# Optimization experiments

Measured on AMD Instinct MI355X. Metric: run time of the kernel, lower is better.

The kernel has to match this reference:

```python
import jax, jax.numpy as jnp
import numpy as np
import math

NUM_CLASSES = 100000
EMBED = 384
BATCH = 512
S = 64.0
M = 0.5
COS_M = math.cos(M)
SIN_M = math.sin(M)
TH = math.cos(math.pi - M)
MM = math.sin(math.pi - M) * M
EPS = 1e-07


def setup_inputs() -> dict:
    key = jax.random.key(0)
    k1, k2, k3 = jax.random.split(key, 3)
    embeddings = jax.random.normal(k1, (BATCH, EMBED), dtype=jnp.float32)
    labels = jax.random.randint(k2, (BATCH,), 0, NUM_CLASSES, dtype=jnp.int64)
    # xavier_uniform-like init for weight [num_classes, embedding_size]
    limit = math.sqrt(6.0 / (NUM_CLASSES + EMBED))
    weight = jax.random.uniform(k3, (NUM_CLASSES, EMBED), dtype=jnp.float32,
                                minval=-limit, maxval=limit)
    return {"embeddings": embeddings, "labels": labels, "weight": weight}


def reference(embeddings, labels, weight):
    # normalize class weights (note: embeddings are NOT normalized, per source)
    W = weight / jnp.linalg.norm(weight, axis=1, keepdims=True)  # [C, E]
    cos_theta = jnp.clip(embeddings @ W.T, -1.0 + EPS, 1.0 - EPS)  # [B, C]
    sin_theta = jnp.sqrt(1.0 - cos_theta ** 2)
    cos_theta_m = cos_theta * COS_M - sin_theta * SIN_M
    cos_theta_m = jnp.where(cos_theta > TH, cos_theta_m, cos_theta - MM)
    one_hot = jax.nn.one_hot(labels, cos_theta.shape[1], dtype=cos_theta.dtype)
    logits = S * (one_hot * cos_theta_m + (1.0 - one_hot) * cos_theta)
    # mean cross-entropy
    logp = jax.nn.log_softmax(logits, axis=-1)  # [B, C]
    nll = -jnp.take_along_axis(logp, labels[:, None], axis=1)[:, 0]
    return jnp.mean(nll)
```

## Files before the change

### kernel.cpp

```cpp
#include <hip/hip_runtime.h>
#include <hip/hip_bf16.h>
#include <math.h>

#define C_CLASSES 100000
#define EMBED     384
#define BATCH     512
#define S_SCALE   64.0f
#define COS_M_    0.8775825618903728f
#define SIN_M_    0.479425538604203f
#define TH_       (-0.8775825618903728f)
#define MM_       0.2397127693021015f
#define EPS_      1e-7f
#define LOG2E_    1.4426950408889634f
#define LN2_      0.6931471805599453f
#define BIGZ_     92.33261191693459f
#define SK1_      92.33248f

#define CT    160
#define NCH   625

typedef __attribute__((ext_vector_type(8))) short bf16x8;
typedef __attribute__((ext_vector_type(4))) float f32x4;

__device__ inline ushort f2bf(float f) {
    unsigned u = __float_as_uint(f);
    unsigned r = (u + 0x7fffu + ((u >> 16) & 1u)) >> 16;
    return (ushort)r;
}

__device__ inline ushort cvt_bf(float f) {
    __hip_bfloat16 h = __float2bfloat16(f);
    return *(ushort*)&h;
}

__global__ __launch_bounds__(256)
void cvt_pack_e(const float* __restrict__ emb, ushort* __restrict__ eP)
{
    int t = blockIdx.x * 256 + threadIdx.x;
    int lane = t & 63;
    int grp  = t >> 6;
    int tile = grp / 12, ks = grp % 12;
    int lr = lane & 15, lg = lane >> 4;
    int row = tile * 16 + lr;
    int col = ks * 32 + lg * 8;
    const float4* src = (const float4*)(emb + (size_t)row * EMBED + col);
    float4 v0 = src[0], v1 = src[1];
    ushort4 o0, o1;
    o0.x = f2bf(v0.x); o0.y = f2bf(v0.y); o0.z = f2bf(v0.z); o0.w = f2bf(v0.w);
    o1.x = f2bf(v1.x); o1.y = f2bf(v1.y); o1.z = f2bf(v1.z); o1.w = f2bf(v1.w);
    ((ushort4*)eP)[t * 2]     = o0;
    ((ushort4*)eP)[t * 2 + 1] = o1;
}

__global__ __launch_bounds__(1024, 4)
void arc_fused160(const ushort* __restrict__ eP, const int* __restrict__ labels,
                  const float* __restrict__ weight,
                  float* __restrict__ psum, float* __restrict__ zlabel)
{
    __shared__ ushort Bl[(CT / 16) * 12 * 512];
    __shared__ int    labL[BATCH];

    const int tid = threadIdx.x;

    const int orig = blockIdx.x;
    const int xcd  = orig & 7;
    const int qq   = NCH >> 3, rr = NCH & 7;
    const int blk  = (xcd < rr ? xcd * (qq + 1)
                               : rr * (qq + 1) + (xcd - rr) * qq) + (orig >> 3);
    const int c0   = blk * CT;

    if (tid < BATCH) labL[tid] = labels[tid];

    {
        const int p = tid & 15;
        #pragma unroll
        for (int h = 0; h < 3; ++h) {
            if (h < 2 || tid < 512) {
                const int c = h * 64 + (tid >> 4);
                const float4* src =
                    (const float4*)(weight + (size_t)(c0 + c) * EMBED) + p;

                float4 wv[6];
                float ss = 0.f;
                #pragma unroll
                for (int i = 0; i < 6; ++i) {
                    wv[i] = src[16 * i];
                    ss += wv[i].x * wv[i].x + wv[i].y * wv[i].y
                        + wv[i].z * wv[i].z + wv[i].w * wv[i].w;
                }
                ss += __shfl_xor(ss, 1, 64);
                ss += __shfl_xor(ss, 2, 64);
                ss += __shfl_xor(ss, 4, 64);
                ss += __shfl_xor(ss, 8, 64);
                const float inv = (ss > 0.f) ? rsqrtf(ss) : 0.f;

                const int t2 = c >> 4, cl = c & 15;
                #pragma unroll
                for (int i = 0; i < 6; ++i) {
                    int q   = p + 16 * i;
                    int ks  = q >> 3;
                    int lgp = (q >> 1) & 3;
                    int jo  = (q & 1) * 4;
                    ushort4 o;
                    o.x = cvt_bf(wv[i].x * inv); o.y = cvt_bf(wv[i].y * inv);
                    o.z = cvt_bf(wv[i].z * inv); o.w = cvt_bf(wv[i].w * inv);
                    int ei = (((t2 * 12 + ks) * 64) + cl + 16 * lgp) * 8 + jo;
                    ei ^= (lgp & 3) << 4;
                    *(ushort4*)&Bl[ei] = o;
                }
            }
            __builtin_amdgcn_sched_barrier(0);
        }
    }
    __syncthreads();

    const int wid = tid >> 6, l = tid & 63;
    const int lr  = l & 15,  lg = l >> 4;
    const int bxo = (lg & 3) << 4;

    const ushort* abase = eP + ((size_t)(wid * 2) * 12 * 64 + l) * 8;

    f32x4 acc[2][10];
    #pragma unroll
    for (int mt = 0; mt < 2; ++mt)
        #pragma unroll
        for (int nt = 0; nt < 10; ++nt)
            acc[mt][nt] = (f32x4){0.f, 0.f, 0.f, 0.f};

    #pragma unroll
    for (int ks = 0; ks < 12; ++ks) {
        bf16x8 a0 = *(const bf16x8*)(abase + (0 * 12 + ks) * 512);
        bf16x8 a1 = *(const bf16x8*)(abase + (1 * 12 + ks) * 512);
        #pragma unroll
        for (int nt = 0; nt < 10; ++nt) {
            int ei = ((nt * 12 + ks) * 64 + l) * 8;
            bf16x8 b = *(const bf16x8*)&Bl[ei ^ bxo];
            acc[0][nt] = __builtin_amdgcn_mfma_f32_16x16x32_bf16(
                a0, b, acc[0][nt], 0, 0, 0);
            acc[1][nt] = __builtin_amdgcn_mfma_f32_16x16x32_bf16(
                a1, b, acc[1][nt], 0, 0, 0);
        }
    }

    #pragma unroll
    for (int mt = 0; mt < 2; ++mt) {
        #pragma unroll
        for (int rg = 0; rg < 4; ++rg) {
            const int r   = wid * 32 + mt * 16 + lg * 4 + rg;
            const int lab = labL[r];
            float acc4 = 0.f;
            #pragma unroll
            for (int nt = 0; nt < 10; ++nt) {
                float cv = __builtin_amdgcn_fmed3f(acc[mt][nt][rg],
                                                   -1.f + EPS_, 1.f - EPS_);
                acc4 += exp2f(fmaf(cv, SK1_, -BIGZ_));
            }
            int off = lab - c0;
            if (((unsigned)off < (unsigned)CT) && ((off & 15) == lr)) {
                int ntl = off >> 4;
                float cv = acc[mt][0][rg];
                #pragma unroll
                for (int nt = 1; nt < 10; ++nt)
                    cv = (ntl == nt) ? acc[mt][nt][rg] : cv;
                cv = __builtin_amdgcn_fmed3f(cv, -1.f + EPS_, 1.f - EPS_);
                float plain = exp2f(fmaf(cv, SK1_, -BIGZ_));
                float zm;
                if (cv > TH_) {
                    float sv = sqrtf(fmaxf(1.f - cv * cv, 0.f));
                    zm = S_SCALE * (cv * COS_M_ - sv * SIN_M_);
                } else {
                    zm = S_SCALE * (cv - MM_);
                }
                acc4 += exp2f(fmaf(zm, LOG2E_, -BIGZ_)) - plain;
                zlabel[r] = zm;
            }
            acc4 += __shfl_xor(acc4, 1, 64);
            acc4 += __shfl_xor(acc4, 2, 64);
            acc4 += __shfl_xor(acc4, 4, 64);
            acc4 += __shfl_xor(acc4, 8, 64);
            if (lr == 0) psum[(size_t)blk * BATCH + r] = acc4;
        }
    }
}

__global__ __launch_bounds__(256)
void arc_reduce(const float* __restrict__ psum, const float* __restrict__ zlabel,
                float* __restrict__ rowloss)
{
    const int r = blockIdx.x;
    const int tid = threadIdx.x;
    float s = 0.f;
    for (int k = tid; k < NCH; k += 256)
        s += psum[(size_t)k * BATCH + r];
    #pragma unroll
    for (int d = 1; d < 64; d <<= 1) s += __shfl_xor(s, d, 64);
    __shared__ float ssh[4];
    if ((tid & 63) == 0) ssh[tid >> 6] = s;
    __syncthreads();
    if (tid == 0) {
        float t = ssh[0] + ssh[1] + ssh[2] + ssh[3];
        rowloss[r] = LN2_ * (BIGZ_ + log2f(t)) - zlabel[r];
    }
}

__global__ __launch_bounds__(512)
void arc_mean(const float* __restrict__ rowloss, float* __restrict__ out)
{
    const int tid = threadIdx.x;
    float v = rowloss[tid];
    #pragma unroll
    for (int d = 1; d < 64; d <<= 1) v += __shfl_xor(v, d, 64);
    __shared__ float sv[8];
    if ((tid & 63) == 0) sv[tid >> 6] = v;
    __syncthreads();
    if (tid == 0) {
        float t = 0.f;
        #pragma unroll
        for (int w = 0; w < 8; ++w) t += sv[w];
        out[0] = t / (float)BATCH;
    }
}

extern "C" void kernel_launch(void* const* d_in, const int* in_sizes, int n_in,
                              void* d_out, int out_size, void* d_ws, size_t ws_size,
                              hipStream_t stream)
{
    (void)in_sizes; (void)n_in; (void)out_size; (void)ws_size;
    const float* emb    = (const float*)d_in[0];
    const int*   labels = (const int*)d_in[1];
    const float* weight = (const float*)d_in[2];
    float* out = (float*)d_out;

    float*  psum    = (float*)d_ws;
    float*  zlabel  = psum + (size_t)NCH * BATCH;
    float*  rowloss = zlabel + BATCH;
    ushort* eP      = (ushort*)(rowloss + BATCH);

    cvt_pack_e<<<(BATCH * EMBED / 8) / 256, 256, 0, stream>>>(emb, eP);
    arc_fused160<<<NCH, 1024, 0, stream>>>(eP, labels, weight, psum, zlabel);
    arc_reduce<<<BATCH, 256, 0, stream>>>(psum, zlabel, rowloss);
    arc_mean<<<1, 512, 0, stream>>>(rowloss, out);
}
```

Before: 84.67 us.

## Retile per-wave MFMA work to 64 rows by 80 classes with split partial sums

Each of the 16 waves now computes a 64x80 tile (4 M-tiles by 5 N-tiles) instead of 32x160 (2 by 10). Each LDS B fragment is reused across four A fragments, which halves LDS reads per MFMA. The cost is twice as many global A loads per wave. The split over classes doubles the partial-sum buffer, so the reduce kernel now reads twice as many partials per row.

```diff
diff --git a/kernel.cpp b/kernel.cpp
--- a/kernel.cpp
+++ b/kernel.cpp
@@ -115,52 +115,57 @@
     __syncthreads();
 
     const int wid = tid >> 6, l = tid & 63;
+    const int mg  = wid & 7;
+    const int nh  = wid >> 3;
     const int lr  = l & 15,  lg = l >> 4;
     const int bxo = (lg & 3) << 4;
 
-    const ushort* abase = eP + ((size_t)(wid * 2) * 12 * 64 + l) * 8;
-
-    f32x4 acc[2][10];
-    #pragma unroll
-    for (int mt = 0; mt < 2; ++mt)
-        #pragma unroll
-        for (int nt = 0; nt < 10; ++nt)
+    const ushort* abase = eP + ((size_t)(mg * 4) * 12 * 64 + l) * 8;
+
+    f32x4 acc[4][5];
+    #pragma unroll
+    for (int mt = 0; mt < 4; ++mt)
+        #pragma unroll
+        for (int nt = 0; nt < 5; ++nt)
             acc[mt][nt] = (f32x4){0.f, 0.f, 0.f, 0.f};
 
     #pragma unroll
     for (int ks = 0; ks < 12; ++ks) {
-        bf16x8 a0 = *(const bf16x8*)(abase + (0 * 12 + ks) * 512);
-        bf16x8 a1 = *(const bf16x8*)(abase + (1 * 12 + ks) * 512);
-        #pragma unroll
-        for (int nt = 0; nt < 10; ++nt) {
-            int ei = ((nt * 12 + ks) * 64 + l) * 8;
+        bf16x8 a[4];
+        #pragma unroll
+        for (int mt = 0; mt < 4; ++mt)
+            a[mt] = *(const bf16x8*)(abase + (mt * 12 + ks) * 512);
+        #pragma unroll
+        for (int nt = 0; nt < 5; ++nt) {
+            int ei = (((nh * 5 + nt) * 12 + ks) * 64 + l) * 8;
             bf16x8 b = *(const bf16x8*)&Bl[ei ^ bxo];
-            acc[0][nt] = __builtin_amdgcn_mfma_f32_16x16x32_bf16(
-                a0, b, acc[0][nt], 0, 0, 0);
-            acc[1][nt] = __builtin_amdgcn_mfma_f32_16x16x32_bf16(
-                a1, b, acc[1][nt], 0, 0, 0);
+            #pragma unroll
+            for (int mt = 0; mt < 4; ++mt)
+                acc[mt][nt] = __builtin_amdgcn_mfma_f32_16x16x32_bf16(
+                    a[mt], b, acc[mt][nt], 0, 0, 0);
         }
     }
 
-    #pragma unroll
-    for (int mt = 0; mt < 2; ++mt) {
+    const int cbase = c0 + nh * 80;
+    #pragma unroll
+    for (int mt = 0; mt < 4; ++mt) {
         #pragma unroll
         for (int rg = 0; rg < 4; ++rg) {
-            const int r   = wid * 32 + mt * 16 + lg * 4 + rg;
+            const int r   = mg * 64 + mt * 16 + lg * 4 + rg;
             const int lab = labL[r];
             float acc4 = 0.f;
             #pragma unroll
-            for (int nt = 0; nt < 10; ++nt) {
+            for (int nt = 0; nt < 5; ++nt) {
                 float cv = __builtin_amdgcn_fmed3f(acc[mt][nt][rg],
                                                    -1.f + EPS_, 1.f - EPS_);
                 acc4 += exp2f(fmaf(cv, SK1_, -BIGZ_));
             }
-            int off = lab - c0;
-            if (((unsigned)off < (unsigned)CT) && ((off & 15) == lr)) {
+            int off = lab - cbase;
+            if (((unsigned)off < 80u) && ((off & 15) == lr)) {
                 int ntl = off >> 4;
                 float cv = acc[mt][0][rg];
                 #pragma unroll
-                for (int nt = 1; nt < 10; ++nt)
+                for (int nt = 1; nt < 5; ++nt)
                     cv = (ntl == nt) ? acc[mt][nt][rg] : cv;
                 cv = __builtin_amdgcn_fmed3f(cv, -1.f + EPS_, 1.f - EPS_);
                 float plain = exp2f(fmaf(cv, SK1_, -BIGZ_));
@@ -178,7 +183,8 @@
             acc4 += __shfl_xor(acc4, 2, 64);
             acc4 += __shfl_xor(acc4, 4, 64);
             acc4 += __shfl_xor(acc4, 8, 64);
-            if (lr == 0) psum[(size_t)blk * BATCH + r] = acc4;
+            if (lr == 0)
+                psum[((size_t)blk * 2 + nh) * BATCH + r] = acc4;
         }
     }
 }
@@ -190,7 +196,7 @@
     const int r = blockIdx.x;
     const int tid = threadIdx.x;
     float s = 0.f;
-    for (int k = tid; k < NCH; k += 256)
+    for (int k = tid; k < 2 * NCH; k += 256)
         s += psum[(size_t)k * BATCH + r];
     #pragma unroll
     for (int d = 1; d < 64; d <<= 1) s += __shfl_xor(s, d, 64);
@@ -232,7 +238,7 @@
     float* out = (float*)d_out;
 
     float*  psum    = (float*)d_ws;
-    float*  zlabel  = psum + (size_t)NCH * BATCH;
+    float*  zlabel  = psum + (size_t)2 * NCH * BATCH;
     float*  rowloss = zlabel + BATCH;
     ushort* eP      = (ushort*)(rowloss + BATCH);
 
```

After: 121.1 us. +43.1%, slower.

## Pipeline weight loading with MFMA passes over class-tile groups

Applied to the files above, without the earlier changes.

Splits the 160-class tile into three groups of 64/64/32 classes. While the MFMA pass runs on the group already staged in LDS, the next group's weights are loaded from global memory and then normalised and packed afterward, with a barrier between stages. The aim is to hide weight-load latency behind matrix compute instead of loading all weights before any MFMA work starts. The cost is extra barriers, shorter MFMA passes and register pressure from holding prefetched weights alongside the accumulators.

```diff
diff --git a/kernel.cpp b/kernel.cpp
--- a/kernel.cpp
+++ b/kernel.cpp
@@ -52,93 +52,77 @@
     ((ushort4*)eP)[t * 2 + 1] = o1;
 }
 
-__global__ __launch_bounds__(1024, 4)
-void arc_fused160(const ushort* __restrict__ eP, const int* __restrict__ labels,
-                  const float* __restrict__ weight,
-                  float* __restrict__ psum, float* __restrict__ zlabel)
-{
-    __shared__ ushort Bl[(CT / 16) * 12 * 512];
-    __shared__ int    labL[BATCH];
-
-    const int tid = threadIdx.x;
-
-    const int orig = blockIdx.x;
-    const int xcd  = orig & 7;
-    const int qq   = NCH >> 3, rr = NCH & 7;
-    const int blk  = (xcd < rr ? xcd * (qq + 1)
-                               : rr * (qq + 1) + (xcd - rr) * qq) + (orig >> 3);
-    const int c0   = blk * CT;
-
-    if (tid < BATCH) labL[tid] = labels[tid];
-
-    {
+__device__ __forceinline__ void load_w(const float* __restrict__ weight,
+                                       int c0, int h, int tid, float4 wv[6])
+{
+    if (h < 2 || tid < 512) {
+        const int c = h * 64 + (tid >> 4);
+        const float4* s = (const float4*)(weight + (size_t)(c0 + c) * EMBED)
+                        + (tid & 15);
+        wv[0] = s[0];  wv[1] = s[16]; wv[2] = s[32];
+        wv[3] = s[48]; wv[4] = s[64]; wv[5] = s[80];
+    }
+}
+
+__device__ __forceinline__ void pack_w(ushort* __restrict__ Bl,
+                                       int h, int tid, const float4 wv[6])
+{
+    if (h < 2 || tid < 512) {
+        const int c = h * 64 + (tid >> 4);
         const int p = tid & 15;
-        #pragma unroll
-        for (int h = 0; h < 3; ++h) {
-            if (h < 2 || tid < 512) {
-                const int c = h * 64 + (tid >> 4);
-                const float4* src =
-                    (const float4*)(weight + (size_t)(c0 + c) * EMBED) + p;
-
-                float4 wv[6];
-                float ss = 0.f;
-                #pragma unroll
-                for (int i = 0; i < 6; ++i) {
-                    wv[i] = src[16 * i];
-                    ss += wv[i].x * wv[i].x + wv[i].y * wv[i].y
-                        + wv[i].z * wv[i].z + wv[i].w * wv[i].w;
-                }
-                ss += __shfl_xor(ss, 1, 64);
-                ss += __shfl_xor(ss, 2, 64);
-                ss += __shfl_xor(ss, 4, 64);
-                ss += __shfl_xor(ss, 8, 64);
-                const float inv = (ss > 0.f) ? rsqrtf(ss) : 0.f;
-
-                const int t2 = c >> 4, cl = c & 15;
-                #pragma unroll
-                for (int i = 0; i < 6; ++i) {
-                    int q   = p + 16 * i;
-                    int ks  = q >> 3;
-                    int lgp = (q >> 1) & 3;
-                    int jo  = (q & 1) * 4;
-                    ushort4 o;
-                    o.x = cvt_bf(wv[i].x * inv); o.y = cvt_bf(wv[i].y * inv);
-                    o.z = cvt_bf(wv[i].z * inv); o.w = cvt_bf(wv[i].w * inv);
-                    int ei = (((t2 * 12 + ks) * 64) + cl + 16 * lgp) * 8 + jo;
-                    ei ^= (lgp & 3) << 4;
-                    *(ushort4*)&Bl[ei] = o;
-                }
-            }
-            __builtin_amdgcn_sched_barrier(0);
-        }
-    }
-    __syncthreads();
-
-    const int wid = tid >> 6, l = tid & 63;
-    const int lr  = l & 15,  lg = l >> 4;
-    const int bxo = (lg & 3) << 4;
-
-    const ushort* abase = eP + ((size_t)(wid * 2) * 12 * 64 + l) * 8;
-
-    f32x4 acc[2][10];
+        float ss = 0.f;
+        #pragma unroll
+        for (int i = 0; i < 6; ++i)
+            ss += wv[i].x * wv[i].x + wv[i].y * wv[i].y
+                + wv[i].z * wv[i].z + wv[i].w * wv[i].w;
+        ss += __shfl_xor(ss, 1, 64);
+        ss += __shfl_xor(ss, 2, 64);
+        ss += __shfl_xor(ss, 4, 64);
+        ss += __shfl_xor(ss, 8, 64);
+        const float inv = (ss > 0.f) ? rsqrtf(ss) : 0.f;
+        const int t2 = c >> 4, cl = c & 15;
+        #pragma unroll
+        for (int i = 0; i < 6; ++i) {
+            int q   = p + 16 * i;
+            int ks  = q >> 3;
+            int lgp = (q >> 1) & 3;
+            int jo  = (q & 1) * 4;
+            ushort4 o;
+            o.x = cvt_bf(wv[i].x * inv); o.y = cvt_bf(wv[i].y * inv);
+            o.z = cvt_bf(wv[i].z * inv); o.w = cvt_bf(wv[i].w * inv);
+            int ei = (((t2 * 12 + ks) * 64) + cl + 16 * lgp) * 8 + jo;
+            ei ^= (lgp & 3) << 4;
+            *(ushort4*)&Bl[ei] = o;
+        }
+    }
+}
+
+template<int BASE, int GSZ>
+__device__ __forceinline__ void mfma_pass(
+    const ushort* __restrict__ abase, const ushort* __restrict__ Bl,
+    int bxo, int l, int lr, int lg, int wid, int c0,
+    const int* __restrict__ labL, float zsum[2][4],
+    float* __restrict__ zlabel)
+{
+    f32x4 acc[2][GSZ];
     #pragma unroll
     for (int mt = 0; mt < 2; ++mt)
         #pragma unroll
-        for (int nt = 0; nt < 10; ++nt)
-            acc[mt][nt] = (f32x4){0.f, 0.f, 0.f, 0.f};
+        for (int j = 0; j < GSZ; ++j)
+            acc[mt][j] = (f32x4){0.f, 0.f, 0.f, 0.f};
 
     #pragma unroll
     for (int ks = 0; ks < 12; ++ks) {
         bf16x8 a0 = *(const bf16x8*)(abase + (0 * 12 + ks) * 512);
         bf16x8 a1 = *(const bf16x8*)(abase + (1 * 12 + ks) * 512);
         #pragma unroll
-        for (int nt = 0; nt < 10; ++nt) {
-            int ei = ((nt * 12 + ks) * 64 + l) * 8;
+        for (int j = 0; j < GSZ; ++j) {
+            int ei = (((BASE + j) * 12 + ks) * 64 + l) * 8;
             bf16x8 b = *(const bf16x8*)&Bl[ei ^ bxo];
-            acc[0][nt] = __builtin_amdgcn_mfma_f32_16x16x32_bf16(
-                a0, b, acc[0][nt], 0, 0, 0);
-            acc[1][nt] = __builtin_amdgcn_mfma_f32_16x16x32_bf16(
-                a1, b, acc[1][nt], 0, 0, 0);
+            acc[0][j] = __builtin_amdgcn_mfma_f32_16x16x32_bf16(
+                a0, b, acc[0][j], 0, 0, 0);
+            acc[1][j] = __builtin_amdgcn_mfma_f32_16x16x32_bf16(
+                a1, b, acc[1][j], 0, 0, 0);
         }
     }
 
@@ -148,20 +132,21 @@
         for (int rg = 0; rg < 4; ++rg) {
             const int r   = wid * 32 + mt * 16 + lg * 4 + rg;
             const int lab = labL[r];
-            float acc4 = 0.f;
+            float s = 0.f;
             #pragma unroll
-            for (int nt = 0; nt < 10; ++nt) {
-                float cv = __builtin_amdgcn_fmed3f(acc[mt][nt][rg],
+            for (int j = 0; j < GSZ; ++j) {
+                float cv = __builtin_amdgcn_fmed3f(acc[mt][j][rg],
                                                    -1.f + EPS_, 1.f - EPS_);
-                acc4 += exp2f(fmaf(cv, SK1_, -BIGZ_));
+                s += exp2f(fmaf(cv, SK1_, -BIGZ_));
             }
-            int off = lab - c0;
-            if (((unsigned)off < (unsigned)CT) && ((off & 15) == lr)) {
+            zsum[mt][rg] += s;
+            int off = lab - (c0 + BASE * 16);
+            if (((unsigned)off < (unsigned)(GSZ * 16)) && ((off & 15) == lr)) {
                 int ntl = off >> 4;
                 float cv = acc[mt][0][rg];
                 #pragma unroll
-                for (int nt = 1; nt < 10; ++nt)
-                    cv = (ntl == nt) ? acc[mt][nt][rg] : cv;
+                for (int j = 1; j < GSZ; ++j)
+                    cv = (ntl == j) ? acc[mt][j][rg] : cv;
                 cv = __builtin_amdgcn_fmed3f(cv, -1.f + EPS_, 1.f - EPS_);
                 float plain = exp2f(fmaf(cv, SK1_, -BIGZ_));
                 float zm;
@@ -171,14 +156,74 @@
                 } else {
                     zm = S_SCALE * (cv - MM_);
                 }
-                acc4 += exp2f(fmaf(zm, LOG2E_, -BIGZ_)) - plain;
+                zsum[mt][rg] += exp2f(fmaf(zm, LOG2E_, -BIGZ_)) - plain;
                 zlabel[r] = zm;
             }
-            acc4 += __shfl_xor(acc4, 1, 64);
-            acc4 += __shfl_xor(acc4, 2, 64);
-            acc4 += __shfl_xor(acc4, 4, 64);
-            acc4 += __shfl_xor(acc4, 8, 64);
-            if (lr == 0) psum[(size_t)blk * BATCH + r] = acc4;
+        }
+    }
+}
+
+__global__ __launch_bounds__(1024, 4)
+void arc_pipe160(const ushort* __restrict__ eP, const int* __restrict__ labels,
+                 const float* __restrict__ weight,
+                 float* __restrict__ psum, float* __restrict__ zlabel)
+{
+    __shared__ ushort Bl[(CT / 16) * 12 * 512];
+    __shared__ int    labL[BATCH];
+
+    const int tid = threadIdx.x;
+
+    const int orig = blockIdx.x;
+    const int xcd  = orig & 7;
+    const int qq   = NCH >> 3, rr = NCH & 7;
+    const int blk  = (xcd < rr ? xcd * (qq + 1)
+                               : rr * (qq + 1) + (xcd - rr) * qq) + (orig >> 3);
+    const int c0   = blk * CT;
+
+    if (tid < BATCH) labL[tid] = labels[tid];
+
+    const int wid = tid >> 6, l = tid & 63;
+    const int lr  = l & 15,  lg = l >> 4;
+    const int bxo = (lg & 3) << 4;
+    const ushort* abase = eP + ((size_t)(wid * 2) * 12 * 64 + l) * 8;
+
+    float zsum[2][4];
+    #pragma unroll
+    for (int mt = 0; mt < 2; ++mt)
+        #pragma unroll
+        for (int rg = 0; rg < 4; ++rg) zsum[mt][rg] = 0.f;
+
+    float4 wv[6];
+
+    load_w(weight, c0, 0, tid, wv);
+    pack_w(Bl, 0, tid, wv);
+    __syncthreads();
+
+    load_w(weight, c0, 1, tid, wv);
+    __builtin_amdgcn_sched_barrier(0);
+    mfma_pass<0, 4>(abase, Bl, bxo, l, lr, lg, wid, c0, labL, zsum, zlabel);
+    pack_w(Bl, 1, tid, wv);
+    __syncthreads();
+
+    load_w(weight, c0, 2, tid, wv);
+    __builtin_amdgcn_sched_barrier(0);
+    mfma_pass<4, 4>(abase, Bl, bxo, l, lr, lg, wid, c0, labL, zsum, zlabel);
+    pack_w(Bl, 2, tid, wv);
+    __syncthreads();
+
+    mfma_pass<8, 2>(abase, Bl, bxo, l, lr, lg, wid, c0, labL, zsum, zlabel);
+
+    #pragma unroll
+    for (int mt = 0; mt < 2; ++mt) {
+        #pragma unroll
+        for (int rg = 0; rg < 4; ++rg) {
+            const int r = wid * 32 + mt * 16 + lg * 4 + rg;
+            float s = zsum[mt][rg];
+            s += __shfl_xor(s, 1, 64);
+            s += __shfl_xor(s, 2, 64);
+            s += __shfl_xor(s, 4, 64);
+            s += __shfl_xor(s, 8, 64);
+            if (lr == 0) psum[(size_t)blk * BATCH + r] = s;
         }
     }
 }
@@ -237,7 +282,7 @@
     ushort* eP      = (ushort*)(rowloss + BATCH);
 
     cvt_pack_e<<<(BATCH * EMBED / 8) / 256, 256, 0, stream>>>(emb, eP);
-    arc_fused160<<<NCH, 1024, 0, stream>>>(eP, labels, weight, psum, zlabel);
+    arc_pipe160<<<NCH, 1024, 0, stream>>>(eP, labels, weight, psum, zlabel);
     arc_reduce<<<BATCH, 256, 0, stream>>>(psum, zlabel, rowloss);
     arc_mean<<<1, 512, 0, stream>>>(rowloss, out);
 }
```

Measured after the change: 108.7 us. 28.4% more time.

## Split class tiles into full-size and half-size kernels to balance wave tail

Applied to the files above, without the earlier changes.

Processes the first 81920 classes with 512 blocks of 160 classes and the remaining classes with a new kernel using 226 blocks of 80 classes. The goal is to replace the partial third wave of full-size blocks with a wave of smaller blocks, shortening the tail. It adds a second kernel launch and the smaller blocks reuse each embedding load over fewer classes.

```diff
diff --git a/kernel.cpp b/kernel.cpp
--- a/kernel.cpp
+++ b/kernel.cpp
@@ -16,8 +16,10 @@
 #define BIGZ_     92.33261191693459f
 #define SK1_      92.33248f
 
-#define CT    160
-#define NCH   625
+#define NCHA   512
+#define CB_    81920
+#define NCHB   226
+#define NPART  (NCHA + NCHB)
 
 typedef __attribute__((ext_vector_type(8))) short bf16x8;
 typedef __attribute__((ext_vector_type(4))) float f32x4;
@@ -57,17 +59,14 @@
                   const float* __restrict__ weight,
                   float* __restrict__ psum, float* __restrict__ zlabel)
 {
-    __shared__ ushort Bl[(CT / 16) * 12 * 512];
+    __shared__ ushort Bl[10 * 12 * 512];
     __shared__ int    labL[BATCH];
 
     const int tid = threadIdx.x;
 
     const int orig = blockIdx.x;
-    const int xcd  = orig & 7;
-    const int qq   = NCH >> 3, rr = NCH & 7;
-    const int blk  = (xcd < rr ? xcd * (qq + 1)
-                               : rr * (qq + 1) + (xcd - rr) * qq) + (orig >> 3);
-    const int c0   = blk * CT;
+    const int blk  = (orig & 7) * (NCHA >> 3) + (orig >> 3);
+    const int c0   = blk * 160;
 
     if (tid < BATCH) labL[tid] = labels[tid];
 
@@ -156,7 +155,7 @@
                 acc4 += exp2f(fmaf(cv, SK1_, -BIGZ_));
             }
             int off = lab - c0;
-            if (((unsigned)off < (unsigned)CT) && ((off & 15) == lr)) {
+            if (((unsigned)off < 160u) && ((off & 15) == lr)) {
                 int ntl = off >> 4;
                 float cv = acc[mt][0][rg];
                 #pragma unroll
@@ -183,6 +182,129 @@
     }
 }
 
+__global__ __launch_bounds__(1024, 4)
+void arc_fused80(const ushort* __restrict__ eP, const int* __restrict__ labels,
+                 const float* __restrict__ weight,
+                 float* __restrict__ psum, float* __restrict__ zlabel)
+{
+    __shared__ ushort Bl[5 * 12 * 512];
+    __shared__ int    labL[BATCH];
+
+    const int tid = threadIdx.x;
+
+    const int orig = blockIdx.x;
+    const int xcd  = orig & 7;
+    const int qq   = NCHB >> 3, rr = NCHB & 7;
+    const int blk  = (xcd < rr ? xcd * (qq + 1)
+                               : rr * (qq + 1) + (xcd - rr) * qq) + (orig >> 3);
+    const int c0   = CB_ + blk * 80;
+
+    if (tid < BATCH) labL[tid] = labels[tid];
+
+    if (tid < 640) {
+        const int c = tid >> 3;
+        const int p = tid & 7;
+        const float4* src = (const float4*)(weight + (size_t)(c0 + c) * EMBED) + p;
+
+        float4 wv[12];
+        float ss = 0.f;
+        #pragma unroll
+        for (int i = 0; i < 12; ++i) {
+            wv[i] = src[8 * i];
+            ss += wv[i].x * wv[i].x + wv[i].y * wv[i].y
+                + wv[i].z * wv[i].z + wv[i].w * wv[i].w;
+        }
+        ss += __shfl_xor(ss, 1, 64);
+        ss += __shfl_xor(ss, 2, 64);
+        ss += __shfl_xor(ss, 4, 64);
+        const float inv = (ss > 0.f) ? rsqrtf(ss) : 0.f;
+
+        const int t2 = c >> 4, cl = c & 15;
+        #pragma unroll
+        for (int i = 0; i < 12; ++i) {
+            int q   = p + 8 * i;
+            int ks  = q >> 3;
+            int lgp = (q >> 1) & 3;
+            int jo  = (q & 1) * 4;
+            ushort4 o;
+            o.x = cvt_bf(wv[i].x * inv); o.y = cvt_bf(wv[i].y * inv);
+            o.z = cvt_bf(wv[i].z * inv); o.w = cvt_bf(wv[i].w * inv);
+            int ei = (((t2 * 12 + ks) * 64) + cl + 16 * lgp) * 8 + jo;
+            ei ^= (lgp & 3) << 4;
+            *(ushort4*)&Bl[ei] = o;
+        }
+    }
+    __syncthreads();
+
+    const int wid = tid >> 6, l = tid & 63;
+    const int lr  = l & 15,  lg = l >> 4;
+    const int bxo = (lg & 3) << 4;
+
+    const ushort* abase = eP + ((size_t)(wid * 2) * 12 * 64 + l) * 8;
+
+    f32x4 acc[2][5];
+    #pragma unroll
+    for (int mt = 0; mt < 2; ++mt)
+        #pragma unroll
+        for (int nt = 0; nt < 5; ++nt)
+            acc[mt][nt] = (f32x4){0.f, 0.f, 0.f, 0.f};
+
+    #pragma unroll
+    for (int ks = 0; ks < 12; ++ks) {
+        bf16x8 a0 = *(const bf16x8*)(abase + (0 * 12 + ks) * 512);
+        bf16x8 a1 = *(const bf16x8*)(abase + (1 * 12 + ks) * 512);
+        #pragma unroll
+        for (int nt = 0; nt < 5; ++nt) {
+            int ei = ((nt * 12 + ks) * 64 + l) * 8;
+            bf16x8 b = *(const bf16x8*)&Bl[ei ^ bxo];
+            acc[0][nt] = __builtin_amdgcn_mfma_f32_16x16x32_bf16(
+                a0, b, acc[0][nt], 0, 0, 0);
+            acc[1][nt] = __builtin_amdgcn_mfma_f32_16x16x32_bf16(
+                a1, b, acc[1][nt], 0, 0, 0);
+        }
+    }
+
+    #pragma unroll
+    for (int mt = 0; mt < 2; ++mt) {
+        #pragma unroll
+        for (int rg = 0; rg < 4; ++rg) {
+            const int r   = wid * 32 + mt * 16 + lg * 4 + rg;
+            const int lab = labL[r];
+            float acc4 = 0.f;
+            #pragma unroll
+            for (int nt = 0; nt < 5; ++nt) {
+                float cv = __builtin_amdgcn_fmed3f(acc[mt][nt][rg],
+                                                   -1.f + EPS_, 1.f - EPS_);
+                acc4 += exp2f(fmaf(cv, SK1_, -BIGZ_));
+            }
+            int off = lab - c0;
+            if (((unsigned)off < 80u) && ((off & 15) == lr)) {
+                int ntl = off >> 4;
+                float cv = acc[mt][0][rg];
+                #pragma unroll
+                for (int nt = 1; nt < 5; ++nt)
+                    cv = (ntl == nt) ? acc[mt][nt][rg] : cv;
+                cv = __builtin_amdgcn_fmed3f(cv, -1.f + EPS_, 1.f - EPS_);
+                float plain = exp2f(fmaf(cv, SK1_, -BIGZ_));
+                float zm;
+                if (cv > TH_) {
+                    float sv = sqrtf(fmaxf(1.f - cv * cv, 0.f));
+                    zm = S_SCALE * (cv * COS_M_ - sv * SIN_M_);
+                } else {
+                    zm = S_SCALE * (cv - MM_);
+                }
+                acc4 += exp2f(fmaf(zm, LOG2E_, -BIGZ_)) - plain;
+                zlabel[r] = zm;
+            }
+            acc4 += __shfl_xor(acc4, 1, 64);
+            acc4 += __shfl_xor(acc4, 2, 64);
+            acc4 += __shfl_xor(acc4, 4, 64);
+            acc4 += __shfl_xor(acc4, 8, 64);
+            if (lr == 0) psum[(size_t)(NCHA + blk) * BATCH + r] = acc4;
+        }
+    }
+}
+
 __global__ __launch_bounds__(256)
 void arc_reduce(const float* __restrict__ psum, const float* __restrict__ zlabel,
                 float* __restrict__ rowloss)
@@ -190,7 +312,7 @@
     const int r = blockIdx.x;
     const int tid = threadIdx.x;
     float s = 0.f;
-    for (int k = tid; k < NCH; k += 256)
+    for (int k = tid; k < NPART; k += 256)
         s += psum[(size_t)k * BATCH + r];
     #pragma unroll
     for (int d = 1; d < 64; d <<= 1) s += __shfl_xor(s, d, 64);
@@ -232,12 +354,13 @@
     float* out = (float*)d_out;
 
     float*  psum    = (float*)d_ws;
-    float*  zlabel  = psum + (size_t)NCH * BATCH;
+    float*  zlabel  = psum + (size_t)NPART * BATCH;
     float*  rowloss = zlabel + BATCH;
     ushort* eP      = (ushort*)(rowloss + BATCH);
 
     cvt_pack_e<<<(BATCH * EMBED / 8) / 256, 256, 0, stream>>>(emb, eP);
-    arc_fused160<<<NCH, 1024, 0, stream>>>(eP, labels, weight, psum, zlabel);
+    arc_fused160<<<NCHA, 1024, 0, stream>>>(eP, labels, weight, psum, zlabel);
+    arc_fused80<<<NCHB, 1024, 0, stream>>>(eP, labels, weight, psum, zlabel);
     arc_reduce<<<BATCH, 256, 0, stream>>>(psum, zlabel, rowloss);
     arc_mean<<<1, 512, 0, stream>>>(rowloss, out);
 }
```

After: 82.75 us. 1.02x faster.
